# Kernel tuning notes

Hardware: AMD Instinct MI355X
Metric: run time of the kernel (lower is better)

The kernel has to match this reference:

```python
import jax, jax.numpy as jnp
import numpy as np

EPS = 1e-6
NUM_HEADS = 16

def _rms(x, w=None):
    y = x * jax.lax.rsqrt(jnp.mean(x * x, axis=-1, keepdims=True) + EPS)
    return y if w is None else y * w

def _rope(q, k, pos):
    # q,k: [B,H,T,Dh]; half-split (rotate_half) RoPE convention, base 10000
    dh = q.shape[-1]
    half = dh // 2
    freqs = 1.0 / (10000.0 ** (jnp.arange(half, dtype=jnp.float32) / half))
    ang = pos.astype(jnp.float32)[:, None] * freqs[None, :]  # [T, half]
    cos = jnp.concatenate([jnp.cos(ang), jnp.cos(ang)], -1)  # [T, Dh]
    sin = jnp.concatenate([jnp.sin(ang), jnp.sin(ang)], -1)
    def rot(v):
        v1, v2 = jnp.split(v, 2, axis=-1)
        return jnp.concatenate([-v2, v1], -1)
    return q * cos + rot(q) * sin, k * cos + rot(k) * sin


def setup_inputs() -> dict:
    key = jax.random.key(0)
    ks = jax.random.split(key, 12)
    B, T, D, H = 2, 2048, 1024, NUM_HEADS
    Dh = D // H
    Hm = 2816  # SwiGLU hidden: multiple_of*ceil(int(2*4*D/3)/256)
    s = lambda fan_in: 1.0 / np.sqrt(fan_in)
    return {
        "x": jax.random.normal(ks[0], (B, T, D), jnp.float32),
        "c": jax.random.normal(ks[1], (B, D), jnp.float32),
        "pos": jnp.arange(T, dtype=jnp.int32),
        "adaln_w": jax.random.normal(ks[2], (D, 6 * D), jnp.float32) * s(D) * 0.1,
        "adaln_b": jax.random.normal(ks[3], (6 * D,), jnp.float32) * 0.02,
        "qkv_w": jax.random.normal(ks[4], (D, 3 * D), jnp.float32) * s(D),
        "lnq_w": jnp.ones((Dh,), jnp.float32),
        "lnk_w": jnp.ones((Dh,), jnp.float32),
        "proj_w": jax.random.normal(ks[5], (D, D), jnp.float32) * s(D),
        "proj_b": jnp.zeros((D,), jnp.float32),
        "w1_w": jax.random.normal(ks[6], (D, Hm), jnp.float32) * s(D),
        "w3_w": jax.random.normal(ks[7], (D, Hm), jnp.float32) * s(D),
        "w2_w": jax.random.normal(ks[8], (Hm, D), jnp.float32) * s(Hm),
    }


def reference(x, c, pos, adaln_w, adaln_b, qkv_w, lnq_w, lnk_w, proj_w, proj_b, w1_w, w3_w, w2_w):
    B, T, D = x.shape
    H = NUM_HEADS
    Dh = D // H

    # AdaLN: SiLU -> Linear -> chunk(6)
    mods = jax.nn.silu(c) @ adaln_w + adaln_b  # [B,6D]
    shift_msa, scale_msa, gate_msa, shift_mlp, scale_mlp, gate_mlp = jnp.split(mods, 6, axis=-1)

    # norm1 (RMSNorm, no affine) + modulate along seq dim
    x_mod = _rms(x) * (1.0 + scale_msa[:, None, :]) + shift_msa[:, None, :]

    # QKV projection (no bias)
    qkv = x_mod @ qkv_w  # [B,T,3D]
    q, k, v = jnp.split(qkv, 3, axis=-1)
    q = q.reshape(B, T, H, Dh).transpose(0, 2, 1, 3)  # [B,H,T,Dh]
    k = k.reshape(B, T, H, Dh).transpose(0, 2, 1, 3)
    v = v.reshape(B, T, H, Dh).transpose(0, 2, 1, 3)

    # per-head RMS qk-norm with affine weight
    q = _rms(q, lnq_w)
    k = _rms(k, lnk_w)

    # 1D RoPE
    q, k = _rope(q, k, pos)

    # attention core (SDPA, delegated in the original module)
    scores = jnp.einsum('bhqd,bhkd->bhqk', q, k) / jnp.sqrt(jnp.float32(Dh))
    attn = jax.nn.softmax(scores, axis=-1)
    attn_out = jnp.einsum('bhqk,bhkd->bhqd', attn, v)  # [B,H,T,Dh]
    attn_out = attn_out.transpose(0, 2, 1, 3).reshape(B, T, D)

    # post_attention: gated residual + SwiGLU MLP
    x = x + gate_msa[:, None, :] * (attn_out @ proj_w + proj_b)
    h = _rms(x) * (1.0 + scale_mlp[:, None, :]) + shift_mlp[:, None, :]
    mlp = (jax.nn.silu(h @ w1_w) * (h @ w3_w)) @ w2_w
    x = x + gate_mlp[:, None, :] * mlp
    return x
```

## Files before the change

kernel.cpp:

```cpp
#include <hip/hip_runtime.h>
#include <stdint.h>
#include <math.h>

typedef unsigned short u16;
typedef __attribute__((ext_vector_type(4))) float f32x4;
typedef __attribute__((ext_vector_type(16))) float f32x16;
typedef __attribute__((ext_vector_type(8))) __bf16 bf16x8;

#define DEV static __device__ __forceinline__

typedef __attribute__((address_space(1))) void gvoid;
typedef __attribute__((address_space(3))) void lvoid;

DEV float bf2f(u16 u){ uint32_t v = ((uint32_t)u) << 16; float f; __builtin_memcpy(&f, &v, 4); return f; }
DEV u16 f2bf(float f){ uint32_t v; __builtin_memcpy(&v, &f, 4); v = (v + 0x7fffu + ((v >> 16) & 1u)) >> 16; return (u16)v; }

DEV void cp16(const void* g, void* l){
  __builtin_amdgcn_global_load_lds((gvoid*)g, (lvoid*)l, 16, 0, 0);
}
DEV f32x4 mfma16(bf16x8 a, bf16x8 b, f32x4 c){
  return __builtin_amdgcn_mfma_f32_16x16x32_bf16(a, b, c, 0, 0, 0);
}
DEV f32x16 mfma32(bf16x8 a, bf16x8 b, f32x16 c){
  return __builtin_amdgcn_mfma_f32_32x32x16_bf16(a, b, c, 0, 0, 0);
}
DEV uint32_t cvtpk(float a, float b){
  uint32_t r;
  asm volatile("v_cvt_pk_bf16_f32 %0, %1, %2" : "=v"(r) : "v"(a), "v"(b));
  return r;
}
DEV void uswap(uint32_t& a, uint32_t& b){
  asm volatile("v_permlane32_swap_b32 %0, %1" : "+v"(a), "+v"(b));
}
DEV void fswap(float& a, float& b){
  asm volatile("v_permlane32_swap_b32 %0, %1" : "+v"(a), "+v"(b));
}
DEV float fexp2(float x){
  float r;
  asm("v_exp_f32 %0, %1" : "=v"(r) : "v"(x));
  return r;
}

__global__ void __launch_bounds__(256) adaln1(const float* __restrict__ c,
                                              const float* __restrict__ w,
                                              float* __restrict__ part)
{
  __shared__ float sc[256];
  int k0 = blockIdx.y * 128;
  {
    int i = threadIdx.x;
    int b = i >> 7, kk = i & 127;
    float v = c[b * 1024 + k0 + kk];
    sc[i] = v / (1.f + __expf(-v));
  }
  __syncthreads();
  int col = blockIdx.x * 256 + threadIdx.x;
  float a0 = 0.f, a1 = 0.f;
  #pragma unroll 8
  for (int k = 0; k < 128; ++k){
    float wv = w[(size_t)(k0 + k) * 6144 + col];
    a0 += sc[k] * wv;
    a1 += sc[128 + k] * wv;
  }
  part[((size_t)blockIdx.y * 2 + 0) * 6144 + col] = a0;
  part[((size_t)blockIdx.y * 2 + 1) * 6144 + col] = a1;
}

__global__ void __launch_bounds__(256) adaln2(const float* __restrict__ part,
                                              const float* __restrict__ bias,
                                              float* __restrict__ mods)
{
  int i = blockIdx.x * 256 + threadIdx.x;
  int b = i / 6144, col = i % 6144;
  float a = bias[col];
  #pragma unroll
  for (int r = 0; r < 8; ++r) a += part[((size_t)r * 2 + b) * 6144 + col];
  mods[i] = a;
}

__global__ void __launch_bounds__(256) rope_table(const int* __restrict__ pos,
                                                  float* __restrict__ ct,
                                                  float* __restrict__ st)
{
  int idx = blockIdx.x * 256 + threadIdx.x;
  int t = idx >> 5, i = idx & 31;
  float freq = expf(-0.28782313662425575f * (float)i);
  float ang = (float)pos[t] * freq;
  ct[idx] = cosf(ang);
  st[idx] = sinf(ang);
}

__global__ void __launch_bounds__(256) rmsmod(const float* __restrict__ x,
                                              const float* __restrict__ mods,
                                              u16* __restrict__ out,
                                              int shift_off, int scale_off)
{
  __shared__ float wsum[4];
  int row = blockIdx.x;
  int b = row >> 11;
  const float4 v = ((const float4*)(x + (size_t)row * 1024))[threadIdx.x];
  float ss = v.x * v.x + v.y * v.y + v.z * v.z + v.w * v.w;
  #pragma unroll
  for (int m = 1; m < 64; m <<= 1) ss += __shfl_xor(ss, m);
  if ((threadIdx.x & 63) == 0) wsum[threadIdx.x >> 6] = ss;
  __syncthreads();
  float tot = wsum[0] + wsum[1] + wsum[2] + wsum[3];
  float rr = rsqrtf(tot * (1.f / 1024.f) + 1e-6f);
  const float* mb = mods + (size_t)b * 6144;
  int d0 = threadIdx.x * 4;
  ushort4 o;
  o.x = f2bf(v.x * rr * (1.f + mb[scale_off + d0 + 0]) + mb[shift_off + d0 + 0]);
  o.y = f2bf(v.y * rr * (1.f + mb[scale_off + d0 + 1]) + mb[shift_off + d0 + 1]);
  o.z = f2bf(v.z * rr * (1.f + mb[scale_off + d0 + 2]) + mb[shift_off + d0 + 2]);
  o.w = f2bf(v.w * rr * (1.f + mb[scale_off + d0 + 3]) + mb[shift_off + d0 + 3]);
  ((ushort4*)(out + (size_t)row * 1024))[threadIdx.x] = o;
}

__global__ void __launch_bounds__(256) transpose_w(const float* __restrict__ in,
                                                   u16* __restrict__ out, int R, int C)
{
  __shared__ float t[32][33];
  int tx = threadIdx.x & 31, ty = threadIdx.x >> 5;
  int c0 = blockIdx.x * 32, r0 = blockIdx.y * 32;
  #pragma unroll
  for (int i = 0; i < 4; ++i) t[ty + 8 * i][tx] = in[(size_t)(r0 + ty + 8 * i) * C + c0 + tx];
  __syncthreads();
  #pragma unroll
  for (int i = 0; i < 4; ++i) out[(size_t)(c0 + ty + 8 * i) * R + r0 + tx] = f2bf(t[tx][ty + 8 * i]);
}

__global__ void __launch_bounds__(256) vtrans(const u16* __restrict__ qkv,
                                              u16* __restrict__ vt)
{
  __shared__ u16 tile[32][33];
  int tx = threadIdx.x & 31, ty = threadIdx.x >> 5;
  int t0 = blockIdx.x * 32;
  int d0 = blockIdx.y * 32;
  int bh = blockIdx.z; int b = bh >> 4, h = bh & 15;
  #pragma unroll
  for (int i = 0; i < 4; ++i) {
    int t = t0 + ty + 8 * i;
    tile[ty + 8 * i][tx] = qkv[((size_t)(b * 2048 + t)) * 3072 + 2048 + h * 64 + d0 + tx];
  }
  __syncthreads();
  #pragma unroll
  for (int i = 0; i < 4; ++i) {
    int d = d0 + ty + 8 * i;
    vt[((size_t)bh * 64 + d) * 2048 + t0 + tx] = tile[tx][ty + 8 * i];
  }
}

__global__ void __launch_bounds__(256) gemm_bt(const u16* __restrict__ A,
                                               const u16* __restrict__ Bt,
                                               int M, int N, int K,
                                               u16* __restrict__ outb)
{
  __shared__ __align__(16) u16 Ash[128 * 64];
  __shared__ __align__(16) u16 Bsh[128 * 64];
  const int tid = threadIdx.x;
  const int l = tid & 63, w = tid >> 6;
  const int nwg = gridDim.x * gridDim.y;
  const int id = blockIdx.y * gridDim.x + blockIdx.x;
  const int nid = (id & 7) * (nwg >> 3) + (id >> 3);
  const int bx = nid % gridDim.x, by = nid / gridDim.x;
  const int m0 = by * 128, n0 = bx * 128;
  const int wr = (w >> 1) * 64, wc = (w & 1) * 64;
  const int fr = l & 15, fg = l >> 4;
  const int sw = fr & 7;
  f32x4 acc[4][4] = {};

  for (int kt = 0; kt < K; kt += 64) {
    __syncthreads();
    #pragma unroll
    for (int p = 0; p < 4; ++p) {
      int slot = p * 256 + tid;
      int r = slot >> 3, kp = slot & 7;
      int kpg = kp ^ (r & 7);
      cp16(A + (size_t)(m0 + r) * K + kt + kpg * 8, Ash + slot * 8);
      cp16(Bt + (size_t)(n0 + r) * K + kt + kpg * 8, Bsh + slot * 8);
    }
    __syncthreads();
    #pragma unroll
    for (int kk = 0; kk < 2; ++kk) {
      const int coff = ((kk * 4 + fg) ^ sw) * 8;
      bf16x8 af[4], bfr[4];
      #pragma unroll
      for (int m = 0; m < 4; ++m) af[m] = *(const bf16x8*)(Ash + (wr + m * 16 + fr) * 64 + coff);
      #pragma unroll
      for (int n = 0; n < 4; ++n) bfr[n] = *(const bf16x8*)(Bsh + (wc + n * 16 + fr) * 64 + coff);
      #pragma unroll
      for (int m = 0; m < 4; ++m)
        #pragma unroll
        for (int n = 0; n < 4; ++n)
          acc[m][n] = mfma16(af[m], bfr[n], acc[m][n]);
    }
  }

  #pragma unroll
  for (int m = 0; m < 4; ++m)
  #pragma unroll
  for (int n = 0; n < 4; ++n)
  #pragma unroll
  for (int j = 0; j < 4; ++j) {
    int row = m0 + wr + m * 16 + fg * 4 + j;
    int col = n0 + wc + n * 16 + fr;
    outb[(size_t)row * N + col] = f2bf(acc[m][n][j]);
  }
}

template<int EPI>
__global__ void __launch_bounds__(256) gemm_skinny(const u16* __restrict__ A,
                                                   const u16* __restrict__ Bt,
                                                   int M, int N, int K,
                                                   const float* __restrict__ mods,
                                                   int gate_off,
                                                   const float* __restrict__ bias,
                                                   const float* __restrict__ res,
                                                   float* __restrict__ outf)
{
  __shared__ __align__(16) u16 Ash[2][64 * 64];
  __shared__ __align__(16) u16 Bsh[2][128 * 64];
  const int tid = threadIdx.x;
  const int l = tid & 63, w = tid >> 6;
  const int nwg = gridDim.x * gridDim.y;
  const int id = blockIdx.y * gridDim.x + blockIdx.x;
  const int nid = (id & 7) * (nwg >> 3) + (id >> 3);
  const int bx = nid % gridDim.x, by = nid / gridDim.x;
  const int m0 = by * 64, n0 = bx * 128;
  const int wr = (w >> 1) * 32, wc = (w & 1) * 64;
  const int fr = l & 15, fg = l >> 4;
  const int sw = fr & 7;
  const int nk = K >> 6;
  f32x4 acc[2][4] = {};

  auto stage = [&](int kt, int bsel) {
    #pragma unroll
    for (int p = 0; p < 2; ++p) {
      int slot = p * 256 + tid;
      int r = slot >> 3, kp = slot & 7;
      int kpg = kp ^ (r & 7);
      cp16(A + (size_t)(m0 + r) * K + kt + kpg * 8, &Ash[bsel][slot * 8]);
    }
    #pragma unroll
    for (int p = 0; p < 4; ++p) {
      int slot = p * 256 + tid;
      int r = slot >> 3, kp = slot & 7;
      int kpg = kp ^ (r & 7);
      cp16(Bt + (size_t)(n0 + r) * K + kt + kpg * 8, &Bsh[bsel][slot * 8]);
    }
  };

  stage(0, 0);
  __syncthreads();

  for (int t = 0; t < nk; ++t) {
    if (t + 1 < nk) stage((t + 1) << 6, (t + 1) & 1);
    const u16* Ab = Ash[t & 1];
    const u16* Bb = Bsh[t & 1];
    #pragma unroll
    for (int kk = 0; kk < 2; ++kk) {
      const int coff = ((kk * 4 + fg) ^ sw) * 8;
      bf16x8 af[2], bfr[4];
      #pragma unroll
      for (int m = 0; m < 2; ++m) af[m] = *(const bf16x8*)(Ab + (wr + m * 16 + fr) * 64 + coff);
      #pragma unroll
      for (int n = 0; n < 4; ++n) bfr[n] = *(const bf16x8*)(Bb + (wc + n * 16 + fr) * 64 + coff);
      #pragma unroll
      for (int m = 0; m < 2; ++m)
        #pragma unroll
        for (int n = 0; n < 4; ++n)
          acc[m][n] = mfma16(af[m], bfr[n], acc[m][n]);
    }
    __syncthreads();
  }

  #pragma unroll
  for (int m = 0; m < 2; ++m)
  #pragma unroll
  for (int n = 0; n < 4; ++n)
  #pragma unroll
  for (int j = 0; j < 4; ++j) {
    int row = m0 + wr + m * 16 + fg * 4 + j;
    int col = n0 + wc + n * 16 + fr;
    size_t idx = (size_t)row * N + col;
    float v = acc[m][n][j];
    int b = row >> 11;
    if (EPI == 1)
      outf[idx] = res[idx] + mods[(size_t)b * 6144 + gate_off + col] * (v + bias[col]);
    else
      outf[idx] = res[idx] + mods[(size_t)b * 6144 + gate_off + col] * v;
  }
}

__global__ void __launch_bounds__(256) gemm_w13(const u16* __restrict__ A,
                                                const u16* __restrict__ B1t,
                                                const u16* __restrict__ B3t,
                                                u16* __restrict__ outb)
{
  const int K = 1024, N = 2816;
  __shared__ __align__(16) u16 Ash[128 * 64];
  __shared__ __align__(16) u16 B1sh[64 * 64];
  __shared__ __align__(16) u16 B3sh[64 * 64];
  const int tid = threadIdx.x;
  const int l = tid & 63, w = tid >> 6;
  const int nwg = gridDim.x * gridDim.y;
  const int id = blockIdx.y * gridDim.x + blockIdx.x;
  const int nid = (id & 7) * (nwg >> 3) + (id >> 3);
  const int bx = nid % gridDim.x, by = nid / gridDim.x;
  const int m0 = by * 128, n0 = bx * 64;
  const int wr = (w >> 1) * 64, wc = (w & 1) * 32;
  const int fr = l & 15, fg = l >> 4;
  const int sw = fr & 7;
  f32x4 acc1[4][2] = {}, acc3[4][2] = {};

  for (int kt = 0; kt < K; kt += 64) {
    __syncthreads();
    #pragma unroll
    for (int p = 0; p < 4; ++p) {
      int slot = p * 256 + tid;
      int r = slot >> 3, kp = slot & 7;
      int kpg = kp ^ (r & 7);
      cp16(A + (size_t)(m0 + r) * K + kt + kpg * 8, Ash + slot * 8);
    }
    #pragma unroll
    for (int p = 0; p < 2; ++p) {
      int slot = p * 256 + tid;
      int r = slot >> 3, kp = slot & 7;
      int kpg = kp ^ (r & 7);
      cp16(B1t + (size_t)(n0 + r) * K + kt + kpg * 8, B1sh + slot * 8);
      cp16(B3t + (size_t)(n0 + r) * K + kt + kpg * 8, B3sh + slot * 8);
    }
    __syncthreads();
    #pragma unroll
    for (int kk = 0; kk < 2; ++kk) {
      const int coff = ((kk * 4 + fg) ^ sw) * 8;
      bf16x8 af[4], b1f[2], b3f[2];
      #pragma unroll
      for (int m = 0; m < 4; ++m) af[m] = *(const bf16x8*)(Ash + (wr + m * 16 + fr) * 64 + coff);
      #pragma unroll
      for (int n = 0; n < 2; ++n) {
        b1f[n] = *(const bf16x8*)(B1sh + (wc + n * 16 + fr) * 64 + coff);
        b3f[n] = *(const bf16x8*)(B3sh + (wc + n * 16 + fr) * 64 + coff);
      }
      #pragma unroll
      for (int m = 0; m < 4; ++m)
        #pragma unroll
        for (int n = 0; n < 2; ++n) {
          acc1[m][n] = mfma16(af[m], b1f[n], acc1[m][n]);
          acc3[m][n] = mfma16(af[m], b3f[n], acc3[m][n]);
        }
    }
  }

  #pragma unroll
  for (int m = 0; m < 4; ++m)
  #pragma unroll
  for (int n = 0; n < 2; ++n)
  #pragma unroll
  for (int j = 0; j < 4; ++j) {
    int row = m0 + wr + m * 16 + fg * 4 + j;
    int col = n0 + wc + n * 16 + fr;
    float v1 = acc1[m][n][j];
    float v3 = acc3[m][n][j];
    float s = v1 / (1.f + __expf(-v1));
    outb[(size_t)row * N + col] = f2bf(s * v3);
  }
}

__global__ void __launch_bounds__(256) qknorm_rope(const u16* __restrict__ qkv,
                                                   const float* __restrict__ lnq,
                                                   const float* __restrict__ lnk,
                                                   const float* __restrict__ ctab,
                                                   const float* __restrict__ stab,
                                                   u16* __restrict__ qo,
                                                   u16* __restrict__ ko)
{
  int r = blockIdx.x * 4 + (threadIdx.x >> 6);
  int l = threadIdx.x & 63;
  int h = r & 15, t = (r >> 4) & 2047, b = r >> 15;
  const u16* base = qkv + ((size_t)(b * 2048 + t)) * 3072 + h * 64 + l;
  float q = bf2f(base[0]);
  float k = bf2f(base[1024]);
  float sq = q * q, sk = k * k;
  #pragma unroll
  for (int m = 1; m < 64; m <<= 1) { sq += __shfl_xor(sq, m); sk += __shfl_xor(sk, m); }
  float rq = rsqrtf(sq * (1.f / 64.f) + 1e-6f);
  float rk = rsqrtf(sk * (1.f / 64.f) + 1e-6f);
  float yq = q * rq * lnq[l];
  float yk = k * rk * lnk[l];
  float cs = ctab[t * 32 + (l & 31)];
  float sn = stab[t * 32 + (l & 31)];
  float pq = __shfl_xor(yq, 32);
  float pk = __shfl_xor(yk, 32);
  float rotq = (l < 32) ? -pq : pq;
  float rotk = (l < 32) ? -pk : pk;
  float oq = (yq * cs + rotq * sn) * 0.1803368801111204f;
  float ok = yk * cs + rotk * sn;
  size_t oidx = ((size_t)(b * 16 + h) * 2048 + t) * 64 + l;
  qo[oidx] = f2bf(oq);
  ko[oidx] = f2bf(ok);
}

__global__ void __launch_bounds__(256, 2) flash_attn(const u16* __restrict__ qg,
                                                     const u16* __restrict__ kg,
                                                     const u16* __restrict__ vtg,
                                                     u16* __restrict__ og)
{
  __shared__ __align__(16) char smem[65536];
  const int tid = threadIdx.x, l = tid & 63, w = tid >> 6;
  const int lq = l & 31, hi = l >> 5;
  const int swz = lq & 7;
  const int xcd = blockIdx.x & 7, slot = blockIdx.x >> 3;
  const int g = slot >> 4, qt = slot & 15;
  const int bh = g * 8 + xcd;
  const int h = bh & 15, b = bh >> 4;

  bf16x8 qf[4];
  {
    const u16* qp = qg + ((size_t)bh * 2048 + qt * 128 + w * 32 + lq) * 64 + hi * 8;
    #pragma unroll
    for (int ks = 0; ks < 4; ++ks) qf[ks] = *(const bf16x8*)(qp + ks * 16);
  }
  const u16* kgb = kg + (size_t)bh * 2048 * 64;
  const u16* vgb = vtg + (size_t)bh * 64 * 2048;

  auto stage = [&](int kv, int bsel) {
    #pragma unroll
    for (int p = 0; p < 4; ++p) {
      int s2 = p * 256 + tid;
      int r = s2 >> 3, cl = s2 & 7;
      int cg = cl ^ (r & 7);
      cp16(kgb + (size_t)(kv + r) * 64 + cg * 8, smem + bsel * 16384 + s2 * 16);
    }
    #pragma unroll
    for (int p = 0; p < 4; ++p) {
      int s2 = p * 256 + tid;
      int r = s2 >> 4, cl = s2 & 15;
      int cg = cl ^ (r & 7);
      cp16(vgb + (size_t)r * 2048 + kv + cg * 8, smem + 32768 + bsel * 16384 + s2 * 16);
    }
  };

  f32x16 ob0 = {}, ob1 = {};
  float l_run = 0.f;

  stage(0, 0);
  __syncthreads();

  for (int t = 0; t < 16; ++t) {
    const int cur = t & 1;
    stage(((t + 1) & 15) * 128, cur ^ 1);
    const char* Kb = smem + cur * 16384;
    const char* Vb = smem + 32768 + cur * 16384;

    #pragma unroll
    for (int ko = 0; ko < 128; ko += 64) {
      f32x16 s0 = {}, s1 = {};
      __builtin_amdgcn_s_setprio(1);
      #pragma unroll
      for (int ks = 0; ks < 4; ++ks) {
        const int c = hi + ks * 2;
        bf16x8 kf0 = *(const bf16x8*)(Kb + (ko + lq) * 128 + ((c ^ swz) << 4));
        bf16x8 kf1 = *(const bf16x8*)(Kb + (ko + 32 + lq) * 128 + ((c ^ swz) << 4));
        s0 = mfma32(kf0, qf[ks], s0);
        s1 = mfma32(kf1, qf[ks], s1);
      }
      __builtin_amdgcn_s_setprio(0);
      #pragma unroll
      for (int r = 0; r < 16; ++r) s0[r] = fexp2(s0[r]);
      #pragma unroll
      for (int r = 0; r < 16; ++r) s1[r] = fexp2(s1[r]);
      {
        float t0 = (s0[0] + s0[1]) + (s0[2] + s0[3]);
        float t1 = (s0[4] + s0[5]) + (s0[6] + s0[7]);
        float t2 = (s0[8] + s0[9]) + (s0[10] + s0[11]);
        float t3 = (s0[12] + s0[13]) + (s0[14] + s0[15]);
        float u0 = (s1[0] + s1[1]) + (s1[2] + s1[3]);
        float u1 = (s1[4] + s1[5]) + (s1[6] + s1[7]);
        float u2 = (s1[8] + s1[9]) + (s1[10] + s1[11]);
        float u3 = (s1[12] + s1[13]) + (s1[14] + s1[15]);
        float ls = ((t0 + t1) + (t2 + t3)) + ((u0 + u1) + (u2 + u3));
        float lo = ls;
        fswap(ls, lo);
        l_run += ls + lo;
      }
      uint32_t pw[16];
      {
        uint32_t x0 = cvtpk(s0[0], s0[1]),   y0 = cvtpk(s0[4], s0[5]);   uswap(x0, y0);
        uint32_t x1 = cvtpk(s0[2], s0[3]),   y1 = cvtpk(s0[6], s0[7]);   uswap(x1, y1);
        uint32_t x2 = cvtpk(s0[8], s0[9]),   y2 = cvtpk(s0[12], s0[13]); uswap(x2, y2);
        uint32_t x3 = cvtpk(s0[10], s0[11]), y3 = cvtpk(s0[14], s0[15]); uswap(x3, y3);
        pw[0] = x0; pw[1] = x1; pw[2] = y0; pw[3] = y1;
        pw[4] = x2; pw[5] = x3; pw[6] = y2; pw[7] = y3;
      }
      {
        uint32_t x0 = cvtpk(s1[0], s1[1]),   y0 = cvtpk(s1[4], s1[5]);   uswap(x0, y0);
        uint32_t x1 = cvtpk(s1[2], s1[3]),   y1 = cvtpk(s1[6], s1[7]);   uswap(x1, y1);
        uint32_t x2 = cvtpk(s1[8], s1[9]),   y2 = cvtpk(s1[12], s1[13]); uswap(x2, y2);
        uint32_t x3 = cvtpk(s1[10], s1[11]), y3 = cvtpk(s1[14], s1[15]); uswap(x3, y3);
        pw[8] = x0;  pw[9] = x1;  pw[10] = y0; pw[11] = y1;
        pw[12] = x2; pw[13] = x3; pw[14] = y2; pw[15] = y3;
      }
      __builtin_amdgcn_s_setprio(1);
      #pragma unroll
      for (int ks = 0; ks < 4; ++ks) {
        union { uint32_t u[4]; bf16x8 v; } pk_;
        pk_.u[0] = pw[ks * 4 + 0]; pk_.u[1] = pw[ks * 4 + 1];
        pk_.u[2] = pw[ks * 4 + 2]; pk_.u[3] = pw[ks * 4 + 3];
        const int c = (ko >> 3) + ks * 2 + hi;
        bf16x8 vf0 = *(const bf16x8*)(Vb + lq * 256 + ((c ^ swz) << 4));
        bf16x8 vf1 = *(const bf16x8*)(Vb + (32 + lq) * 256 + ((c ^ swz) << 4));
        ob0 = mfma32(vf0, pk_.v, ob0);
        ob1 = mfma32(vf1, pk_.v, ob1);
      }
      __builtin_amdgcn_s_setprio(0);
    }
    __syncthreads();
  }

  float invl = 1.0f / l_run;
  char* ob_base = smem + w * 4096 + lq * 128 + 8 * hi;
  #pragma unroll
  for (int g2 = 0; g2 < 4; ++g2) {
    uint2 t2;
    t2.x = cvtpk(ob0[g2 * 4 + 0] * invl, ob0[g2 * 4 + 1] * invl);
    t2.y = cvtpk(ob0[g2 * 4 + 2] * invl, ob0[g2 * 4 + 3] * invl);
    *(uint2*)(ob_base + ((g2 ^ (lq & 7)) << 4)) = t2;
    uint2 t3;
    t3.x = cvtpk(ob1[g2 * 4 + 0] * invl, ob1[g2 * 4 + 1] * invl);
    t3.y = cvtpk(ob1[g2 * 4 + 2] * invl, ob1[g2 * 4 + 3] * invl);
    *(uint2*)(ob_base + (((g2 + 4) ^ (lq & 7)) << 4)) = t3;
  }
  __syncthreads();
  #pragma unroll
  for (int i = 0; i < 4; ++i) {
    int idx = i * 256 + tid;
    int ww = idx >> 8, q = (idx >> 3) & 31, s = idx & 7;
    uint4 val = *(const uint4*)(smem + ww * 4096 + q * 128 + ((s ^ (q & 7)) << 4));
    int t = qt * 128 + ww * 32 + q;
    *(uint4*)(og + ((size_t)(b * 2048 + t)) * 1024 + h * 64 + s * 8) = val;
  }
}

extern "C" void kernel_launch(void* const* d_in, const int* in_sizes, int n_in,
                              void* d_out, int out_size, void* d_ws, size_t ws_size,
                              hipStream_t stream)
{
  (void)in_sizes; (void)n_in; (void)out_size; (void)ws_size;
  const float* x       = (const float*)d_in[0];
  const float* c       = (const float*)d_in[1];
  const int*   pos     = (const int*)d_in[2];
  const float* adaln_w = (const float*)d_in[3];
  const float* adaln_b = (const float*)d_in[4];
  const float* qkv_w   = (const float*)d_in[5];
  const float* lnq     = (const float*)d_in[6];
  const float* lnk     = (const float*)d_in[7];
  const float* proj_w  = (const float*)d_in[8];
  const float* proj_b  = (const float*)d_in[9];
  const float* w1_w    = (const float*)d_in[10];
  const float* w3_w    = (const float*)d_in[11];
  const float* w2_w    = (const float*)d_in[12];
  float* out = (float*)d_out;

  char* ws = (char*)d_ws;
  size_t off = 0;
  auto alloc = [&](size_t bytes) -> char* {
    char* p = ws + off; off += (bytes + 255) & ~(size_t)255; return p;
  };
  float* part    = (float*)alloc((size_t)8 * 2 * 6144 * 4);
  float* mods    = (float*)alloc((size_t)2 * 6144 * 4);
  float* ctab    = (float*)alloc((size_t)2048 * 32 * 4);
  float* stab    = (float*)alloc((size_t)2048 * 32 * 4);
  u16* qkv_wt    = (u16*)alloc((size_t)3072 * 1024 * 2);
  u16* proj_wt   = (u16*)alloc((size_t)1024 * 1024 * 2);
  u16* w1_wt     = (u16*)alloc((size_t)2816 * 1024 * 2);
  u16* w3_wt     = (u16*)alloc((size_t)2816 * 1024 * 2);
  u16* w2_wt     = (u16*)alloc((size_t)1024 * 2816 * 2);
  float* x1      = (float*)alloc((size_t)4096 * 1024 * 4);
  u16* attn_bf   = (u16*)alloc((size_t)4096 * 1024 * 2);
  char* pool = ws + off;
  u16* xmod_bf   = (u16*)(pool);
  u16* qkv_bf    = (u16*)(pool + 8388608);
  u16* q_bf      = (u16*)(pool + 33554432);
  u16* k_bf      = (u16*)(pool + 41943040);
  u16* vt_bf     = (u16*)(pool + 50331648);
  u16* h_bf      = (u16*)(pool);
  u16* hidden_bf = (u16*)(pool + 31457280);

  adaln1<<<dim3(24, 8), 256, 0, stream>>>(c, adaln_w, part);
  adaln2<<<48, 256, 0, stream>>>(part, adaln_b, mods);
  rope_table<<<256, 256, 0, stream>>>(pos, ctab, stab);
  rmsmod<<<4096, 256, 0, stream>>>(x, mods, xmod_bf, 0, 1024);
  transpose_w<<<dim3(96, 32), 256, 0, stream>>>(qkv_w, qkv_wt, 1024, 3072);
  transpose_w<<<dim3(32, 32), 256, 0, stream>>>(proj_w, proj_wt, 1024, 1024);
  transpose_w<<<dim3(88, 32), 256, 0, stream>>>(w1_w, w1_wt, 1024, 2816);
  transpose_w<<<dim3(88, 32), 256, 0, stream>>>(w3_w, w3_wt, 1024, 2816);
  transpose_w<<<dim3(32, 88), 256, 0, stream>>>(w2_w, w2_wt, 2816, 1024);

  gemm_bt<<<dim3(24, 32), 256, 0, stream>>>(xmod_bf, qkv_wt, 4096, 3072, 1024, qkv_bf);
  qknorm_rope<<<16384, 256, 0, stream>>>(qkv_bf, lnq, lnk, ctab, stab, q_bf, k_bf);
  vtrans<<<dim3(64, 2, 32), 256, 0, stream>>>(qkv_bf, vt_bf);
  flash_attn<<<512, 256, 0, stream>>>(q_bf, k_bf, vt_bf, attn_bf);
  gemm_skinny<1><<<dim3(8, 64), 256, 0, stream>>>(attn_bf, proj_wt, 4096, 1024, 1024,
                                                  mods, 2048, proj_b, x, x1);
  rmsmod<<<4096, 256, 0, stream>>>(x1, mods, h_bf, 3072, 4096);
  gemm_w13<<<dim3(44, 32), 256, 0, stream>>>(h_bf, w1_wt, w3_wt, hidden_bf);
  gemm_skinny<4><<<dim3(8, 64), 256, 0, stream>>>(hidden_bf, w2_wt, 4096, 1024, 2816,
                                                  mods, 5120, nullptr, x1, out);
}
```

Before: 254.1 us.

## Double-buffer LDS in QKV and W13 GEMMs and remap workgroups into per-XCD slabs

Converts gemm_bt and gemm_w13 from single-buffered LDS tiles with two barriers per K step to double-buffered tiles, where the next K tile is prefetched while the current one is computed. This is meant to overlap global-to-LDS loads with MFMA work. It also adds a slab-based block remap, used by all three GEMM kernels, that gives each XCD (block id mod 8) a contiguous 2D slab of output tiles to improve L2 reuse. The cost is doubled LDS use, which may lower occupancy, most of all in gemm_bt at 64 KB.

Measured after the change: 270.4 us. 1.06x slower.

```diff
diff --git a/kernel.cpp b/kernel.cpp
--- a/kernel.cpp
+++ b/kernel.cpp
@@ -39,6 +39,19 @@
   float r;
   asm("v_exp_f32 %0, %1" : "=v"(r) : "v"(x));
   return r;
+}
+
+DEV void slab_remap(int SX, int SY, int& bx, int& by)
+{
+  const int GX = gridDim.x;
+  const int h = blockIdx.y * GX + blockIdx.x;
+  const int x = h & 7, s = h >> 3;
+  const int ssz = SX * SY;
+  const int nsx = GX / SX;
+  const int slab = x + 8 * (s / ssz);
+  const int ws = s % ssz;
+  bx = (slab % nsx) * SX + ws % SX;
+  by = (slab / nsx) * SY + ws / SX;
 }
 
 __global__ void __launch_bounds__(256) adaln1(const float* __restrict__ c,
@@ -153,47 +166,54 @@
 __global__ void __launch_bounds__(256) gemm_bt(const u16* __restrict__ A,
                                                const u16* __restrict__ Bt,
                                                int M, int N, int K,
+                                               int SX, int SY,
                                                u16* __restrict__ outb)
 {
-  __shared__ __align__(16) u16 Ash[128 * 64];
-  __shared__ __align__(16) u16 Bsh[128 * 64];
+  __shared__ __align__(16) u16 Ash[2][128 * 64];
+  __shared__ __align__(16) u16 Bsh[2][128 * 64];
   const int tid = threadIdx.x;
   const int l = tid & 63, w = tid >> 6;
-  const int nwg = gridDim.x * gridDim.y;
-  const int id = blockIdx.y * gridDim.x + blockIdx.x;
-  const int nid = (id & 7) * (nwg >> 3) + (id >> 3);
-  const int bx = nid % gridDim.x, by = nid / gridDim.x;
+  int bx, by; slab_remap(SX, SY, bx, by);
   const int m0 = by * 128, n0 = bx * 128;
   const int wr = (w >> 1) * 64, wc = (w & 1) * 64;
   const int fr = l & 15, fg = l >> 4;
   const int sw = fr & 7;
+  const int nk = K >> 6;
   f32x4 acc[4][4] = {};
 
-  for (int kt = 0; kt < K; kt += 64) {
-    __syncthreads();
+  auto stage = [&](int kt, int bsel) {
     #pragma unroll
     for (int p = 0; p < 4; ++p) {
       int slot = p * 256 + tid;
       int r = slot >> 3, kp = slot & 7;
       int kpg = kp ^ (r & 7);
-      cp16(A + (size_t)(m0 + r) * K + kt + kpg * 8, Ash + slot * 8);
-      cp16(Bt + (size_t)(n0 + r) * K + kt + kpg * 8, Bsh + slot * 8);
-    }
-    __syncthreads();
+      cp16(A + (size_t)(m0 + r) * K + kt + kpg * 8, &Ash[bsel][slot * 8]);
+      cp16(Bt + (size_t)(n0 + r) * K + kt + kpg * 8, &Bsh[bsel][slot * 8]);
+    }
+  };
+
+  stage(0, 0);
+  __syncthreads();
+
+  for (int t = 0; t < nk; ++t) {
+    if (t + 1 < nk) stage((t + 1) << 6, (t + 1) & 1);
+    const u16* Ab = Ash[t & 1];
+    const u16* Bb = Bsh[t & 1];
     #pragma unroll
     for (int kk = 0; kk < 2; ++kk) {
       const int coff = ((kk * 4 + fg) ^ sw) * 8;
       bf16x8 af[4], bfr[4];
       #pragma unroll
-      for (int m = 0; m < 4; ++m) af[m] = *(const bf16x8*)(Ash + (wr + m * 16 + fr) * 64 + coff);
-      #pragma unroll
-      for (int n = 0; n < 4; ++n) bfr[n] = *(const bf16x8*)(Bsh + (wc + n * 16 + fr) * 64 + coff);
+      for (int m = 0; m < 4; ++m) af[m] = *(const bf16x8*)(Ab + (wr + m * 16 + fr) * 64 + coff);
+      #pragma unroll
+      for (int n = 0; n < 4; ++n) bfr[n] = *(const bf16x8*)(Bb + (wc + n * 16 + fr) * 64 + coff);
       #pragma unroll
       for (int m = 0; m < 4; ++m)
         #pragma unroll
         for (int n = 0; n < 4; ++n)
           acc[m][n] = mfma16(af[m], bfr[n], acc[m][n]);
     }
+    __syncthreads();
   }
 
   #pragma unroll
@@ -222,10 +242,7 @@
   __shared__ __align__(16) u16 Bsh[2][128 * 64];
   const int tid = threadIdx.x;
   const int l = tid & 63, w = tid >> 6;
-  const int nwg = gridDim.x * gridDim.y;
-  const int id = blockIdx.y * gridDim.x + blockIdx.x;
-  const int nid = (id & 7) * (nwg >> 3) + (id >> 3);
-  const int bx = nid % gridDim.x, by = nid / gridDim.x;
+  int bx, by; slab_remap(2, 16, bx, by);
   const int m0 = by * 64, n0 = bx * 128;
   const int wr = (w >> 1) * 32, wc = (w & 1) * 64;
   const int fr = l & 15, fg = l >> 4;
@@ -298,49 +315,54 @@
                                                 u16* __restrict__ outb)
 {
   const int K = 1024, N = 2816;
-  __shared__ __align__(16) u16 Ash[128 * 64];
-  __shared__ __align__(16) u16 B1sh[64 * 64];
-  __shared__ __align__(16) u16 B3sh[64 * 64];
+  __shared__ __align__(16) u16 Ash[2][128 * 64];
+  __shared__ __align__(16) u16 B1sh[2][64 * 64];
+  __shared__ __align__(16) u16 B3sh[2][64 * 64];
   const int tid = threadIdx.x;
   const int l = tid & 63, w = tid >> 6;
-  const int nwg = gridDim.x * gridDim.y;
-  const int id = blockIdx.y * gridDim.x + blockIdx.x;
-  const int nid = (id & 7) * (nwg >> 3) + (id >> 3);
-  const int bx = nid % gridDim.x, by = nid / gridDim.x;
+  int bx, by; slab_remap(11, 8, bx, by);
   const int m0 = by * 128, n0 = bx * 64;
   const int wr = (w >> 1) * 64, wc = (w & 1) * 32;
   const int fr = l & 15, fg = l >> 4;
   const int sw = fr & 7;
   f32x4 acc1[4][2] = {}, acc3[4][2] = {};
 
-  for (int kt = 0; kt < K; kt += 64) {
-    __syncthreads();
+  auto stage = [&](int kt, int bsel) {
     #pragma unroll
     for (int p = 0; p < 4; ++p) {
       int slot = p * 256 + tid;
       int r = slot >> 3, kp = slot & 7;
       int kpg = kp ^ (r & 7);
-      cp16(A + (size_t)(m0 + r) * K + kt + kpg * 8, Ash + slot * 8);
+      cp16(A + (size_t)(m0 + r) * K + kt + kpg * 8, &Ash[bsel][slot * 8]);
     }
     #pragma unroll
     for (int p = 0; p < 2; ++p) {
       int slot = p * 256 + tid;
       int r = slot >> 3, kp = slot & 7;
       int kpg = kp ^ (r & 7);
-      cp16(B1t + (size_t)(n0 + r) * K + kt + kpg * 8, B1sh + slot * 8);
-      cp16(B3t + (size_t)(n0 + r) * K + kt + kpg * 8, B3sh + slot * 8);
-    }
-    __syncthreads();
+      cp16(B1t + (size_t)(n0 + r) * K + kt + kpg * 8, &B1sh[bsel][slot * 8]);
+      cp16(B3t + (size_t)(n0 + r) * K + kt + kpg * 8, &B3sh[bsel][slot * 8]);
+    }
+  };
+
+  stage(0, 0);
+  __syncthreads();
+
+  for (int t = 0; t < 16; ++t) {
+    if (t + 1 < 16) stage((t + 1) << 6, (t + 1) & 1);
+    const u16* Ab  = Ash[t & 1];
+    const u16* B1b = B1sh[t & 1];
+    const u16* B3b = B3sh[t & 1];
     #pragma unroll
     for (int kk = 0; kk < 2; ++kk) {
       const int coff = ((kk * 4 + fg) ^ sw) * 8;
       bf16x8 af[4], b1f[2], b3f[2];
       #pragma unroll
-      for (int m = 0; m < 4; ++m) af[m] = *(const bf16x8*)(Ash + (wr + m * 16 + fr) * 64 + coff);
+      for (int m = 0; m < 4; ++m) af[m] = *(const bf16x8*)(Ab + (wr + m * 16 + fr) * 64 + coff);
       #pragma unroll
       for (int n = 0; n < 2; ++n) {
-        b1f[n] = *(const bf16x8*)(B1sh + (wc + n * 16 + fr) * 64 + coff);
-        b3f[n] = *(const bf16x8*)(B3sh + (wc + n * 16 + fr) * 64 + coff);
+        b1f[n] = *(const bf16x8*)(B1b + (wc + n * 16 + fr) * 64 + coff);
+        b3f[n] = *(const bf16x8*)(B3b + (wc + n * 16 + fr) * 64 + coff);
       }
       #pragma unroll
       for (int m = 0; m < 4; ++m)
@@ -350,6 +372,7 @@
           acc3[m][n] = mfma16(af[m], b3f[n], acc3[m][n]);
         }
     }
+    __syncthreads();
   }
 
   #pragma unroll
@@ -597,7 +620,7 @@
   transpose_w<<<dim3(88, 32), 256, 0, stream>>>(w3_w, w3_wt, 1024, 2816);
   transpose_w<<<dim3(32, 88), 256, 0, stream>>>(w2_w, w2_wt, 2816, 1024);
 
-  gemm_bt<<<dim3(24, 32), 256, 0, stream>>>(xmod_bf, qkv_wt, 4096, 3072, 1024, qkv_bf);
+  gemm_bt<<<dim3(24, 32), 256, 0, stream>>>(xmod_bf, qkv_wt, 4096, 3072, 1024, 6, 8, qkv_bf);
   qknorm_rope<<<16384, 256, 0, stream>>>(qkv_bf, lnq, lnk, ctab, stab, q_bf, k_bf);
   vtrans<<<dim3(64, 2, 32), 256, 0, stream>>>(qkv_bf, vt_bf);
   flash_attn<<<512, 256, 0, stream>>>(q_bf, k_bf, vt_bf, attn_bf);
```
